# Performance work log

Hardware: AMD Instinct MI355X
Metric: run time of the kernel (lower is better)

## Reference

```python
import jax, jax.numpy as jnp
import numpy as np

N, E, F_NODE, F_EDGE, D, OUT, G = 32768, 98304, 32, 16, 64, 16, 64
EPS = 1e-5


def setup_inputs() -> dict:
    key = jax.random.key(0)
    ks = jax.random.split(key, 26)
    s = 0.05
    rn = lambda k, shp: jax.random.normal(k, shp, dtype=jnp.float32) * s
    return {
        "x": jax.random.normal(ks[0], (N, F_NODE), dtype=jnp.float32),
        "edge_attr": jax.random.normal(ks[1], (E, F_EDGE), dtype=jnp.float32),
        "edge_index": jax.random.randint(ks[2], (2, E), 0, N, dtype=jnp.int32),
        "batch": jnp.sort(jax.random.randint(ks[3], (N,), 0, G, dtype=jnp.int32)),
        # fc1
        "fc1_w": rn(ks[4], (F_NODE, D)), "fc1_b": jnp.zeros((D,), jnp.float32),
        # edge MLP 1 + NNConv1 root/bias
        "efc1_w1": rn(ks[5], (F_EDGE, D)), "efc1_b1": jnp.zeros((D,), jnp.float32),
        "efc1_w2": rn(ks[6], (D, D * D)), "efc1_b2": jnp.zeros((D * D,), jnp.float32),
        "root1": rn(ks[7], (D, D)), "bias1": jnp.zeros((D,), jnp.float32),
        "gn1_w": jnp.ones((D,), jnp.float32), "gn1_b": jnp.zeros((D,), jnp.float32),
        # edge MLP 2 + NNConv2 root/bias
        "efc2_w1": rn(ks[8], (F_EDGE, D)), "efc2_b1": jnp.zeros((D,), jnp.float32),
        "efc2_w2": rn(ks[9], (D, D * D)), "efc2_b2": jnp.zeros((D * D,), jnp.float32),
        "root2": rn(ks[10], (D, D)), "bias2": jnp.zeros((D,), jnp.float32),
        "gn2_w": jnp.ones((D,), jnp.float32), "gn2_b": jnp.zeros((D,), jnp.float32),
        # fc2
        "fc2_w": rn(ks[11], (D, OUT)), "fc2_b": jnp.zeros((OUT,), jnp.float32),
    }


def _nnconv(x, edge_index, edge_attr, w1, b1, w2, b2, root, bias):
    # edge MLP -> per-edge [D, D] weight
    h = jax.nn.relu(edge_attr @ w1 + b1)
    we = (h @ w2 + b2).reshape(-1, D, D)          # [E, D, D]
    src, dst = edge_index[0], edge_index[1]
    msg = jnp.einsum('ei,eio->eo', x[src], we)    # per-edge 1xD @ DxD
    agg = jax.ops.segment_sum(msg, dst, num_segments=x.shape[0])  # aggr='add'
    return agg + x @ root + bias


def _graph_layernorm(x, w, b):
    # PyG LayerNorm(mode='graph') with batch=None: global mean/std over all elems
    xc = x - x.mean()
    return xc / (jnp.std(xc) + EPS) * w + b


def _global_mean_pool(h, batch, n_graphs):
    sums = jax.ops.segment_sum(h, batch, num_segments=n_graphs)
    cnt = jax.ops.segment_sum(jnp.ones((h.shape[0],), h.dtype), batch, num_segments=n_graphs)
    return sums / jnp.clip(cnt, 1.0)[:, None]


def reference(x, edge_attr, edge_index, batch,
              fc1_w, fc1_b,
              efc1_w1, efc1_b1, efc1_w2, efc1_b2, root1, bias1, gn1_w, gn1_b,
              efc2_w1, efc2_b1, efc2_w2, efc2_b2, root2, bias2, gn2_w, gn2_b,
              fc2_w, fc2_b):
    hx = x @ fc1_w + fc1_b
    h = jax.nn.relu(_graph_layernorm(
        _nnconv(hx, edge_index, edge_attr, efc1_w1, efc1_b1, efc1_w2, efc1_b2, root1, bias1),
        gn1_w, gn1_b))
    h = jax.nn.relu(_graph_layernorm(
        _nnconv(h, edge_index, edge_attr, efc2_w1, efc2_b1, efc2_w2, efc2_b2, root2, bias2),
        gn2_w, gn2_b))
    pooled = _global_mean_pool(h, batch, G)       # [G, D]
    return pooled @ fc2_w + fc2_b                 # [G, OUT]
```

## Files before the change

### kernel.cpp

```cpp
#include <hip/hip_runtime.h>
#include <hip/hip_bf16.h>
#include <hip/hip_fp16.h>

#define NN    32768
#define EE    98304
#define FN    32
#define FEDGE 16
#define DD    64
#define OUTD  16
#define GG    64
#define EPSL  1e-5f
#define EB    384

typedef __attribute__((ext_vector_type(8))) _Float16 f16x8;
typedef __attribute__((ext_vector_type(4))) float f32x4;

__device__ __forceinline__ void gload_lds16(const void* g, void* l) {
    __builtin_amdgcn_global_load_lds(
        (const __attribute__((address_space(1))) void*)g,
        (__attribute__((address_space(3))) void*)l, 16, 0, 0);
}

__global__ __launch_bounds__(256) void k_fc1agg(const float* __restrict__ x,
                                                const float* __restrict__ w1,
                                                const float* __restrict__ b1,
                                                const float* __restrict__ root,
                                                const float* __restrict__ rbias,
                                                float* __restrict__ hx,
                                                float* __restrict__ agg) {
    __shared__ float rowbuf[4][64];
    int t = threadIdx.x, d = t & 63, wv = t >> 6;
    int n = blockIdx.x * 4 + wv;
    const float* xr = x + n * FN;
    float acc = b1[d];
    #pragma unroll
    for (int i = 0; i < FN; ++i) acc += xr[i] * w1[i * DD + d];
    hx[n * DD + d] = acc;
    rowbuf[wv][d] = acc;
    __syncthreads();
    float a0 = rbias[d], a1 = 0.f, a2 = 0.f, a3 = 0.f;
    #pragma unroll
    for (int i = 0; i < DD; i += 4) {
        a0 += rowbuf[wv][i]     * root[i * DD + d];
        a1 += rowbuf[wv][i + 1] * root[(i + 1) * DD + d];
        a2 += rowbuf[wv][i + 2] * root[(i + 2) * DD + d];
        a3 += rowbuf[wv][i + 3] * root[(i + 3) * DD + d];
    }
    agg[n * DD + d] = (a0 + a1) + (a2 + a3);
}

__global__ __launch_bounds__(256) void k_mlp(const float* __restrict__ ea,
                                             const float* __restrict__ w1,
                                             const float* __restrict__ b1,
                                             __half* __restrict__ het) {
    __shared__ float eas[256][17];
    int t = threadIdx.x;
    int e0 = blockIdx.x * 256;
    const float4* src = (const float4*)(ea + e0 * FEDGE);
    #pragma unroll
    for (int j = 0; j < 4; ++j) {
        float4 v = src[t + 256 * j];
        int f = (t + 256 * j) * 4;
        int e = f >> 4, i = f & 15;
        eas[e][i] = v.x; eas[e][i + 1] = v.y; eas[e][i + 2] = v.z; eas[e][i + 3] = v.w;
    }
    __syncthreads();
    int e = e0 + t;
    float a[FEDGE];
    #pragma unroll
    for (int i = 0; i < FEDGE; ++i) a[i] = eas[t][i];
    for (int k = 0; k < DD; ++k) {
        float acc = b1[k];
        #pragma unroll
        for (int i = 0; i < FEDGE; ++i) acc += a[i] * w1[i * DD + k];
        acc = fmaxf(acc, 0.0f);
        het[k * EE + e] = __float2half_rn(acc);
    }
    het[DD * EE + e] = __float2half_rn(1.0f);
}

__global__ __launch_bounds__(256) void k_prep(const float* __restrict__ w2,
                                              const float* __restrict__ b2,
                                              __half* __restrict__ w2t) {
    int s = blockIdx.x;
    const float* src = (s < 64) ? (w2 + s * 4096) : b2;
    int t = threadIdx.x;
    int o = t >> 2;
    #pragma unroll
    for (int j = 0; j < 16; ++j) {
        int i = (t & 3) * 16 + j;
        w2t[s * 4096 + o * 64 + (i ^ ((o & 7) << 3))] = __float2half_rn(src[i * 64 + o]);
    }
}

__global__ __launch_bounds__(256, 1) void k_conv(const float* __restrict__ xs,
                                                 const __half* __restrict__ het,
                                                 const __half* __restrict__ w2t,
                                                 const int* __restrict__ ei,
                                                 float* __restrict__ agg) {
    __shared__ __align__(16) __half hs[65 * EB];
    __shared__ __align__(16) __half w2s[2 * 4096];

    const int t   = threadIdx.x;
    const int l   = t & 63;
    const int w   = t >> 6;
    const int q   = l >> 4;
    const int r16 = l & 15;
    const int q8  = q * 8;
    const int e0  = blockIdx.x * EB;

    __half2 xh[6][8];
    #pragma unroll
    for (int sm = 0; sm < 6; ++sm) {
        int em = e0 + w * 96 + sm * 16 + r16;
        int sn = ei[em];
        const float4* xr = (const float4*)(xs + sn * DD);
        float4 a0 = xr[q * 2], a1 = xr[q * 2 + 1];
        float4 b0 = xr[8 + q * 2], b1 = xr[8 + q * 2 + 1];
        xh[sm][0] = __floats2half2_rn(a0.x, a0.y);
        xh[sm][1] = __floats2half2_rn(a0.z, a0.w);
        xh[sm][2] = __floats2half2_rn(a1.x, a1.y);
        xh[sm][3] = __floats2half2_rn(a1.z, a1.w);
        xh[sm][4] = __floats2half2_rn(b0.x, b0.y);
        xh[sm][5] = __floats2half2_rn(b0.z, b0.w);
        xh[sm][6] = __floats2half2_rn(b1.x, b1.y);
        xh[sm][7] = __floats2half2_rn(b1.z, b1.w);
    }

    for (int j = t; j < 65 * 48; j += 256) {
        int row = j / 48, col = j - row * 48;
        ((uint4*)hs)[j] = ((const uint4*)(het + row * EE + e0))[col];
    }

    uint boff[2][4];
    #pragma unroll
    for (int nt = 0; nt < 4; ++nt) {
        int o = nt * 16 + r16;
        int xm = (o & 7) << 3;
        #pragma unroll
        for (int p = 0; p < 2; ++p)
            boff[p][nt] = (uint)(o * 64 + ((p * 32 + q8) ^ xm));
    }

    f32x4 acc[6][4];
    #pragma unroll
    for (int sm = 0; sm < 6; ++sm)
        #pragma unroll
        for (int nt = 0; nt < 4; ++nt)
            acc[sm][nt] = (f32x4){0.f, 0.f, 0.f, 0.f};

    auto stage = [&](int s) {
        #pragma unroll
        for (int c = 0; c < 2; ++c)
            gload_lds16(w2t + s * 4096 + w * 1024 + c * 512 + l * 8,
                        &w2s[(s & 1) * 4096 + w * 1024 + c * 512]);
    };

    stage(0);
    asm volatile("s_waitcnt vmcnt(0) lgkmcnt(0)" ::: "memory");

    for (int s = 0; s < 65; ++s) {
        if (s < 64) {
            stage(s + 1);
            asm volatile("s_waitcnt vmcnt(2)" ::: "memory");
        } else {
            asm volatile("s_waitcnt vmcnt(0)" ::: "memory");
        }
        __builtin_amdgcn_s_barrier();
        __builtin_amdgcn_sched_barrier(0);

        const __half* bp = &w2s[(s & 1) * 4096];

        __half2 hh[6];
        #pragma unroll
        for (int sm = 0; sm < 6; ++sm)
            hh[sm] = __half2half2(hs[s * EB + w * 96 + sm * 16 + r16]);

        #pragma unroll
        for (int p = 0; p < 2; ++p) {
            f16x8 bfr[4];
            #pragma unroll
            for (int nt = 0; nt < 4; ++nt)
                bfr[nt] = *(const f16x8*)(bp + boff[p][nt]);
            #pragma unroll
            for (int sm = 0; sm < 6; ++sm) {
                union { f16x8 v; __half2 h2[4]; } af;
                #pragma unroll
                for (int jj = 0; jj < 4; ++jj)
                    af.h2[jj] = __hmul2(hh[sm], xh[sm][p * 4 + jj]);
                #pragma unroll
                for (int nt = 0; nt < 4; ++nt)
                    acc[sm][nt] = __builtin_amdgcn_mfma_f32_16x16x32_f16(
                        af.v, bfr[nt], acc[sm][nt], 0, 0, 0);
            }
        }
        asm volatile("s_waitcnt lgkmcnt(0)" ::: "memory");
        __builtin_amdgcn_s_barrier();
    }

    #pragma unroll
    for (int sm = 0; sm < 6; ++sm) {
        #pragma unroll
        for (int rr = 0; rr < 4; ++rr) {
            int em = e0 + w * 96 + sm * 16 + q * 4 + rr;
            int dn = ei[EE + em];
            float* ar = agg + dn * DD + r16;
            #pragma unroll
            for (int nt = 0; nt < 4; ++nt)
                atomicAdd(ar + nt * 16, acc[sm][nt][rr]);
        }
    }
}

__global__ __launch_bounds__(256) void k_lnred(const float* __restrict__ v,
                                               float* __restrict__ stats) {
    int t = threadIdx.x;
    int base = blockIdx.x * 4096 + t;
    float s = 0.0f, s2 = 0.0f;
    #pragma unroll
    for (int j = 0; j < 16; ++j) {
        float x = v[base + j * 256];
        s += x; s2 += x * x;
    }
    #pragma unroll
    for (int off = 32; off > 0; off >>= 1) {
        s  += __shfl_down(s, off, 64);
        s2 += __shfl_down(s2, off, 64);
    }
    __shared__ float ps[8];
    int w = t >> 6;
    if ((t & 63) == 0) { ps[w] = s; ps[4 + w] = s2; }
    __syncthreads();
    if (t == 0) {
        atomicAdd(&stats[0], ps[0] + ps[1] + ps[2] + ps[3]);
        atomicAdd(&stats[1], ps[4] + ps[5] + ps[6] + ps[7]);
    }
}

__global__ __launch_bounds__(256) void k_lnagg(float* __restrict__ h1,
                                               const float* __restrict__ stats,
                                               const float* __restrict__ gw,
                                               const float* __restrict__ gb,
                                               const float* __restrict__ root,
                                               const float* __restrict__ rbias,
                                               float* __restrict__ agg2) {
    const float M = (float)(NN * DD);
    float mean = stats[0] / M;
    float var  = stats[1] / M - mean * mean;
    float rden = 1.0f / (sqrtf(fmaxf(var, 0.0f)) + EPSL);
    __shared__ float rowbuf[4][64];
    int t = threadIdx.x, d = t & 63, wv = t >> 6;
    int n = blockIdx.x * 4 + wv;
    float v = h1[n * DD + d];
    float h = fmaxf((v - mean) * rden * gw[d] + gb[d], 0.0f);
    h1[n * DD + d] = h;
    rowbuf[wv][d] = h;
    __syncthreads();
    float a0 = rbias[d], a1 = 0.f, a2 = 0.f, a3 = 0.f;
    #pragma unroll
    for (int i = 0; i < DD; i += 4) {
        a0 += rowbuf[wv][i]     * root[i * DD + d];
        a1 += rowbuf[wv][i + 1] * root[(i + 1) * DD + d];
        a2 += rowbuf[wv][i + 2] * root[(i + 2) * DD + d];
        a3 += rowbuf[wv][i + 3] * root[(i + 3) * DD + d];
    }
    agg2[n * DD + d] = (a0 + a1) + (a2 + a3);
}

__global__ __launch_bounds__(256) void k_lnpool(const float* __restrict__ v,
                                                const float* __restrict__ stats,
                                                const float* __restrict__ gw,
                                                const float* __restrict__ gb,
                                                const int* __restrict__ batch,
                                                float* __restrict__ pool,
                                                float* __restrict__ cnt) {
    const float M = (float)(NN * DD);
    float mean = stats[0] / M;
    float var  = stats[1] / M - mean * mean;
    float rden = 1.0f / (sqrtf(fmaxf(var, 0.0f)) + EPSL);
    int t = threadIdx.x;
    int d = t & 63;
    int ln = t >> 6;
    int n0 = blockIdx.x * 256;
    float gwd = gw[d] * rden, gbd = gb[d];
    float s = 0.0f, sc = 0.0f;
    int cur = batch[n0 + ln];
    for (int j = 0; j < 64; ++j) {
        int n = n0 + ln + j * 4;
        int b = batch[n];
        if (b != cur) {
            atomicAdd(&pool[cur * DD + d], s);
            if (d == 0) atomicAdd(&cnt[cur], sc);
            s = 0.0f; sc = 0.0f; cur = b;
        }
        s  += fmaxf((v[n * DD + d] - mean) * gwd + gbd, 0.0f);
        sc += 1.0f;
    }
    atomicAdd(&pool[cur * DD + d], s);
    if (d == 0) atomicAdd(&cnt[cur], sc);
}

__global__ __launch_bounds__(256) void k_fc2(const float* __restrict__ pool,
                                             const float* __restrict__ cnt,
                                             const float* __restrict__ w,
                                             const float* __restrict__ b,
                                             float* __restrict__ out) {
    int t = threadIdx.x;
    int o = t & 15;
    int g0 = t >> 4;
    #pragma unroll
    for (int gg = 0; gg < 4; ++gg) {
        int g = g0 + gg * 16;
        float inv = 1.0f / fmaxf(cnt[g], 1.0f);
        float acc = b[o];
        for (int d = 0; d < DD; ++d)
            acc += pool[g * DD + d] * inv * w[d * OUTD + o];
        out[g * OUTD + o] = acc;
    }
}

extern "C" void kernel_launch(void* const* d_in, const int* in_sizes, int n_in,
                              void* d_out, int out_size, void* d_ws, size_t ws_size,
                              hipStream_t stream) {
    const float* x       = (const float*)d_in[0];
    const float* ea      = (const float*)d_in[1];
    const int*   ei      = (const int*)d_in[2];
    const int*   batch   = (const int*)d_in[3];
    const float* fc1_w   = (const float*)d_in[4];
    const float* fc1_b   = (const float*)d_in[5];
    const float* e1w1    = (const float*)d_in[6];
    const float* e1b1    = (const float*)d_in[7];
    const float* e1w2    = (const float*)d_in[8];
    const float* e1b2    = (const float*)d_in[9];
    const float* root1   = (const float*)d_in[10];
    const float* bias1   = (const float*)d_in[11];
    const float* gn1w    = (const float*)d_in[12];
    const float* gn1b    = (const float*)d_in[13];
    const float* e2w1    = (const float*)d_in[14];
    const float* e2b1    = (const float*)d_in[15];
    const float* e2w2    = (const float*)d_in[16];
    const float* e2b2    = (const float*)d_in[17];
    const float* root2   = (const float*)d_in[18];
    const float* bias2   = (const float*)d_in[19];
    const float* gn2w    = (const float*)d_in[20];
    const float* gn2b    = (const float*)d_in[21];
    const float* fc2_w   = (const float*)d_in[22];
    const float* fc2_b   = (const float*)d_in[23];
    float* out = (float*)d_out;

    char* ws = (char*)d_ws;
    float*  hx    = (float*)(ws);
    float*  agg1  = (float*)(ws + 8388608);
    __half* het   = (__half*)(ws + 16777216);
    __half* w2t   = (__half*)(ws + 29556736);
    float*  pool  = (float*)(ws + 30089216);
    float*  cnt   = (float*)(ws + 30105600);
    float*  stats = (float*)(ws + 30105856);
    float*  agg2  = hx;

    hipMemsetAsync(ws + 30089216, 0, 16384 + 256 + 16, stream);

    k_fc1agg<<<NN / 4, 256, 0, stream>>>(x, fc1_w, fc1_b, root1, bias1, hx, agg1);
    k_mlp<<<EE / 256, 256, 0, stream>>>(ea, e1w1, e1b1, het);
    k_prep<<<65, 256, 0, stream>>>(e1w2, e1b2, w2t);
    k_conv<<<EE / EB, 256, 0, stream>>>(hx, het, w2t, ei, agg1);
    k_lnred<<<(NN * DD) / 4096, 256, 0, stream>>>(agg1, stats);
    k_lnagg<<<NN / 4, 256, 0, stream>>>(agg1, stats, gn1w, gn1b, root2, bias2, agg2);

    k_mlp<<<EE / 256, 256, 0, stream>>>(ea, e2w1, e2b1, het);
    k_prep<<<65, 256, 0, stream>>>(e2w2, e2b2, w2t);
    k_conv<<<EE / EB, 256, 0, stream>>>(agg1, het, w2t, ei, agg2);
    k_lnred<<<(NN * DD) / 4096, 256, 0, stream>>>(agg2, stats + 2);

    k_lnpool<<<NN / 256, 256, 0, stream>>>(agg2, stats + 2, gn2w, gn2b, batch, pool, cnt);
    k_fc2<<<1, 256, 0, stream>>>(pool, cnt, fc2_w, fc2_b, out);
}
```

Measured before the change: 422.3 us.

## Retile edge conv with 2x2 wave split, 4-deep weight pipeline, fuse prep kernels

The per-edge conv kernel now handles 192 edges per block instead of 384. Its four waves split as 2 along the edge dimension and 2 along the output columns, and it allows two blocks per CU. The weight slice is staged into a 4-slot LDS ring, prefetched three slices ahead, with one barrier pair per slice instead of the trailing wait and barrier. The edge-MLP and weight-transpose kernels are merged into one launch, and the memset is replaced by zeroing stats, pool and count inside conv block 0. The aim is more parallelism, better latency hiding and fewer launches, at the cost of each wave reusing the A operand across fewer output columns.

```diff
diff --git a/kernel.cpp b/kernel.cpp
--- a/kernel.cpp
+++ b/kernel.cpp
@@ -10,7 +10,7 @@
 #define OUTD  16
 #define GG    64
 #define EPSL  1e-5f
-#define EB    384
+#define EB    192
 
 typedef __attribute__((ext_vector_type(8))) _Float16 f16x8;
 typedef __attribute__((ext_vector_type(4))) float f32x4;
@@ -49,10 +49,13 @@
     agg[n * DD + d] = (a0 + a1) + (a2 + a3);
 }
 
-__global__ __launch_bounds__(256) void k_mlp(const float* __restrict__ ea,
-                                             const float* __restrict__ w1,
-                                             const float* __restrict__ b1,
-                                             __half* __restrict__ het) {
+__global__ __launch_bounds__(256) void k_mlpprep(const float* __restrict__ ea,
+                                                 const float* __restrict__ w1,
+                                                 const float* __restrict__ b1,
+                                                 __half* __restrict__ het,
+                                                 const float* __restrict__ w2,
+                                                 const float* __restrict__ b2,
+                                                 __half* __restrict__ w2t) {
     __shared__ float eas[256][17];
     int t = threadIdx.x;
     int e0 = blockIdx.x * 256;
@@ -64,6 +67,16 @@
         int e = f >> 4, i = f & 15;
         eas[e][i] = v.x; eas[e][i + 1] = v.y; eas[e][i + 2] = v.z; eas[e][i + 3] = v.w;
     }
+    if (blockIdx.x < 65) {
+        int s = blockIdx.x;
+        const float* psrc = (s < 64) ? (w2 + s * 4096) : b2;
+        int o = t >> 2;
+        #pragma unroll
+        for (int j = 0; j < 16; ++j) {
+            int i = (t & 3) * 16 + j;
+            w2t[s * 4096 + o * 64 + (i ^ ((o & 7) << 3))] = __float2half_rn(psrc[i * 64 + o]);
+        }
+    }
     __syncthreads();
     int e = e0 + t;
     float a[FEDGE];
@@ -79,40 +92,34 @@
     het[DD * EE + e] = __float2half_rn(1.0f);
 }
 
-__global__ __launch_bounds__(256) void k_prep(const float* __restrict__ w2,
-                                              const float* __restrict__ b2,
-                                              __half* __restrict__ w2t) {
-    int s = blockIdx.x;
-    const float* src = (s < 64) ? (w2 + s * 4096) : b2;
-    int t = threadIdx.x;
-    int o = t >> 2;
-    #pragma unroll
-    for (int j = 0; j < 16; ++j) {
-        int i = (t & 3) * 16 + j;
-        w2t[s * 4096 + o * 64 + (i ^ ((o & 7) << 3))] = __float2half_rn(src[i * 64 + o]);
-    }
-}
-
-__global__ __launch_bounds__(256, 1) void k_conv(const float* __restrict__ xs,
+__global__ __launch_bounds__(256, 2) void k_conv(const float* __restrict__ xs,
                                                  const __half* __restrict__ het,
                                                  const __half* __restrict__ w2t,
                                                  const int* __restrict__ ei,
-                                                 float* __restrict__ agg) {
+                                                 float* __restrict__ agg,
+                                                 float* __restrict__ zbuf,
+                                                 int zn) {
     __shared__ __align__(16) __half hs[65 * EB];
-    __shared__ __align__(16) __half w2s[2 * 4096];
+    __shared__ __align__(16) __half w2s[4 * 4096];
 
     const int t   = threadIdx.x;
     const int l   = t & 63;
     const int w   = t >> 6;
+    const int wm  = w & 1;
+    const int wn  = w >> 1;
     const int q   = l >> 4;
     const int r16 = l & 15;
     const int q8  = q * 8;
     const int e0  = blockIdx.x * EB;
 
+    if (blockIdx.x == 0) {
+        for (int i = t; i < zn; i += 256) zbuf[i] = 0.0f;
+    }
+
     __half2 xh[6][8];
     #pragma unroll
     for (int sm = 0; sm < 6; ++sm) {
-        int em = e0 + w * 96 + sm * 16 + r16;
+        int em = e0 + wm * 96 + sm * 16 + r16;
         int sn = ei[em];
         const float4* xr = (const float4*)(xs + sn * DD);
         float4 a0 = xr[q * 2], a1 = xr[q * 2 + 1];
@@ -127,61 +134,62 @@
         xh[sm][7] = __floats2half2_rn(b1.z, b1.w);
     }
 
-    for (int j = t; j < 65 * 48; j += 256) {
-        int row = j / 48, col = j - row * 48;
-        ((uint4*)hs)[j] = ((const uint4*)(het + row * EE + e0))[col];
-    }
-
-    uint boff[2][4];
-    #pragma unroll
-    for (int nt = 0; nt < 4; ++nt) {
-        int o = nt * 16 + r16;
-        int xm = (o & 7) << 3;
-        #pragma unroll
-        for (int p = 0; p < 2; ++p)
-            boff[p][nt] = (uint)(o * 64 + ((p * 32 + q8) ^ xm));
-    }
-
-    f32x4 acc[6][4];
-    #pragma unroll
-    for (int sm = 0; sm < 6; ++sm)
-        #pragma unroll
-        for (int nt = 0; nt < 4; ++nt)
-            acc[sm][nt] = (f32x4){0.f, 0.f, 0.f, 0.f};
-
     auto stage = [&](int s) {
         #pragma unroll
         for (int c = 0; c < 2; ++c)
             gload_lds16(w2t + s * 4096 + w * 1024 + c * 512 + l * 8,
-                        &w2s[(s & 1) * 4096 + w * 1024 + c * 512]);
+                        &w2s[(s & 3) * 4096 + w * 1024 + c * 512]);
     };
 
-    stage(0);
-    asm volatile("s_waitcnt vmcnt(0) lgkmcnt(0)" ::: "memory");
+    stage(0); stage(1); stage(2);
+
+    for (int j = t; j < 65 * 24; j += 256) {
+        int row = j / 24, col = j - row * 24;
+        ((uint4*)hs)[j] = ((const uint4*)(het + row * EE + e0))[col];
+    }
+    asm volatile("s_waitcnt lgkmcnt(0)" ::: "memory");
+
+    uint boff[2][2];
+    #pragma unroll
+    for (int j = 0; j < 2; ++j) {
+        int o = (wn * 2 + j) * 16 + r16;
+        int xm = (o & 7) << 3;
+        #pragma unroll
+        for (int p = 0; p < 2; ++p)
+            boff[p][j] = (uint)(o * 64 + ((p * 32 + q8) ^ xm));
+    }
+
+    f32x4 acc[6][2];
+    #pragma unroll
+    for (int sm = 0; sm < 6; ++sm)
+        #pragma unroll
+        for (int j = 0; j < 2; ++j)
+            acc[sm][j] = (f32x4){0.f, 0.f, 0.f, 0.f};
 
     for (int s = 0; s < 65; ++s) {
-        if (s < 64) {
-            stage(s + 1);
-            asm volatile("s_waitcnt vmcnt(2)" ::: "memory");
+        __builtin_amdgcn_s_barrier();
+        if (s < 62) {
+            stage(s + 3);
+            asm volatile("s_waitcnt vmcnt(6)" ::: "memory");
         } else {
             asm volatile("s_waitcnt vmcnt(0)" ::: "memory");
         }
         __builtin_amdgcn_s_barrier();
         __builtin_amdgcn_sched_barrier(0);
 
-        const __half* bp = &w2s[(s & 1) * 4096];
+        const __half* bp = &w2s[(s & 3) * 4096];
 
         __half2 hh[6];
         #pragma unroll
         for (int sm = 0; sm < 6; ++sm)
-            hh[sm] = __half2half2(hs[s * EB + w * 96 + sm * 16 + r16]);
+            hh[sm] = __half2half2(hs[s * EB + wm * 96 + sm * 16 + r16]);
 
         #pragma unroll
         for (int p = 0; p < 2; ++p) {
-            f16x8 bfr[4];
+            f16x8 bfr[2];
             #pragma unroll
-            for (int nt = 0; nt < 4; ++nt)
-                bfr[nt] = *(const f16x8*)(bp + boff[p][nt]);
+            for (int j = 0; j < 2; ++j)
+                bfr[j] = *(const f16x8*)(bp + boff[p][j]);
             #pragma unroll
             for (int sm = 0; sm < 6; ++sm) {
                 union { f16x8 v; __half2 h2[4]; } af;
@@ -189,25 +197,23 @@
                 for (int jj = 0; jj < 4; ++jj)
                     af.h2[jj] = __hmul2(hh[sm], xh[sm][p * 4 + jj]);
                 #pragma unroll
-                for (int nt = 0; nt < 4; ++nt)
-                    acc[sm][nt] = __builtin_amdgcn_mfma_f32_16x16x32_f16(
-                        af.v, bfr[nt], acc[sm][nt], 0, 0, 0);
+                for (int j = 0; j < 2; ++j)
+                    acc[sm][j] = __builtin_amdgcn_mfma_f32_16x16x32_f16(
+                        af.v, bfr[j], acc[sm][j], 0, 0, 0);
             }
         }
-        asm volatile("s_waitcnt lgkmcnt(0)" ::: "memory");
-        __builtin_amdgcn_s_barrier();
     }
 
     #pragma unroll
     for (int sm = 0; sm < 6; ++sm) {
         #pragma unroll
         for (int rr = 0; rr < 4; ++rr) {
-            int em = e0 + w * 96 + sm * 16 + q * 4 + rr;
+            int em = e0 + wm * 96 + sm * 16 + q * 4 + rr;
             int dn = ei[EE + em];
-            float* ar = agg + dn * DD + r16;
+            float* ar = agg + dn * DD + wn * 32 + r16;
             #pragma unroll
-            for (int nt = 0; nt < 4; ++nt)
-                atomicAdd(ar + nt * 16, acc[sm][nt][rr]);
+            for (int j = 0; j < 2; ++j)
+                atomicAdd(ar + j * 16, acc[sm][j][rr]);
         }
     }
 }
@@ -313,6 +319,7 @@
         int g = g0 + gg * 16;
         float inv = 1.0f / fmaxf(cnt[g], 1.0f);
         float acc = b[o];
+        #pragma unroll
         for (int d = 0; d < DD; ++d)
             acc += pool[g * DD + d] * inv * w[d * OUTD + o];
         out[g * OUTD + o] = acc;
@@ -358,18 +365,14 @@
     float*  stats = (float*)(ws + 30105856);
     float*  agg2  = hx;
 
-    hipMemsetAsync(ws + 30089216, 0, 16384 + 256 + 16, stream);
-
     k_fc1agg<<<NN / 4, 256, 0, stream>>>(x, fc1_w, fc1_b, root1, bias1, hx, agg1);
-    k_mlp<<<EE / 256, 256, 0, stream>>>(ea, e1w1, e1b1, het);
-    k_prep<<<65, 256, 0, stream>>>(e1w2, e1b2, w2t);
-    k_conv<<<EE / EB, 256, 0, stream>>>(hx, het, w2t, ei, agg1);
+    k_mlpprep<<<EE / 256, 256, 0, stream>>>(ea, e1w1, e1b1, het, e1w2, e1b2, w2t);
+    k_conv<<<EE / EB, 256, 0, stream>>>(hx, het, w2t, ei, agg1, stats, 2);
     k_lnred<<<(NN * DD) / 4096, 256, 0, stream>>>(agg1, stats);
     k_lnagg<<<NN / 4, 256, 0, stream>>>(agg1, stats, gn1w, gn1b, root2, bias2, agg2);
 
-    k_mlp<<<EE / 256, 256, 0, stream>>>(ea, e2w1, e2b1, het);
-    k_prep<<<65, 256, 0, stream>>>(e2w2, e2b2, w2t);
-    k_conv<<<EE / EB, 256, 0, stream>>>(agg1, het, w2t, ei, agg2);
+    k_mlpprep<<<EE / 256, 256, 0, stream>>>(ea, e2w1, e2b1, het, e2w2, e2b2, w2t);
+    k_conv<<<EE / EB, 256, 0, stream>>>(agg1, het, w2t, ei, agg2, pool, 4096 + 64 + 4);
     k_lnred<<<(NN * DD) / 4096, 256, 0, stream>>>(agg2, stats + 2);
 
     k_lnpool<<<NN / 256, 256, 0, stream>>>(agg2, stats + 2, gn2w, gn2b, batch, pool, cnt);
```

Result: faster. 386.0 us (-8.6%).
